# Performance work log

Hardware: AMD Instinct MI355X
Metric: run time of the kernel (lower is better)

## Reference

```python
import jax, jax.numpy as jnp
import numpy as np

N, D, HID, G, E2 = 2048, 256, 128, 8, 16384


def _mlp(h, w1, b1, g, be, w2, b2):
    # Linear -> ReLU -> BatchNorm1d (training mode, biased batch var) -> Linear
    h = jax.nn.relu(h @ w1 + b1)
    mu = h.mean(axis=0)
    var = ((h - mu) ** 2).mean(axis=0)
    h = (h - mu) / jnp.sqrt(var + 1e-5) * g + be
    return h @ w2 + b2


def setup_inputs() -> dict:
    key = jax.random.key(0)
    ks = jax.random.split(key, 12)
    x = jax.random.normal(ks[0], (N, D), jnp.float32)
    src = jax.random.randint(ks[1], (E2,), 0, N)
    dst = jax.random.randint(ks[2], (E2,), 0, N)
    src = jnp.where(src == dst, (src + 1) % N, src)  # no self loops
    edge_index = jnp.stack([jnp.concatenate([src, dst]),
                            jnp.concatenate([dst, src])])  # symmetric
    batch = jnp.sort(jax.random.randint(ks[3], (N,), 0, G))
    def lin(k, i, o):
        return 0.1 * jax.random.normal(k, (i, o), jnp.float32)
    out = dict(x=x, edge_index=edge_index, batch=batch)
    dims = [(1, HID, HID), (HID, HID, HID), (HID, HID, 1)]
    names = [("w11", "b11", "g1", "be1", "w12", "b12"),
             ("w21", "b21", "g2", "be2", "w22", "b22"),
             ("w31", "b31", "g3", "be3", "w32", "b32")]
    k = 4
    for (i, h, o), n in zip(dims, names):
        out[n[0]] = lin(ks[k], i, h)
        out[n[1]] = jnp.zeros((h,), jnp.float32)
        out[n[2]] = jnp.ones((h,), jnp.float32)
        out[n[3]] = jnp.zeros((h,), jnp.float32)
        out[n[4]] = lin(ks[k + 1], h, o)
        out[n[5]] = jnp.zeros((o,), jnp.float32)
        k += 2
    return out


def reference(x, edge_index, batch,
              w11, b11, g1, be1, w12, b12,
              w21, b21, g2, be2, w22, b22,
              w31, b31, g3, be3, w32, b32):
    n = x.shape[0]
    # dense adjacency from edge_index; L = D - A (unnormalized graph Laplacian)
    A = jnp.zeros((n, n), x.dtype).at[edge_index[0], edge_index[1]].set(1.0)
    deg = A.sum(axis=1)
    # entropy term: V = x*(Lx) - x*(Ax) + A(x*x), Lx = deg*x - Ax
    Ax = A @ x
    V = x * (deg[:, None] * x - Ax) - x * Ax + A @ (x * x)
    V = jnp.linalg.norm(V, axis=1)  # [n]
    # per-graph softmax over the batch segments
    mx = jax.ops.segment_max(V, batch, num_segments=G)
    ex = jnp.exp(V - mx[batch])
    P = ex / jax.ops.segment_sum(ex, batch, num_segments=G)[batch]
    P = jnp.where(P == 0.0, 1.0, P)
    ent = -P * jnp.log(P)  # [n]

    # GINConv (eps=0): mlp(x + sum_{j in N(i)} x_j) = mlp(x + A @ x)
    def gin(h, w1, b1, g, be, w2, b2):
        return _mlp(h + A @ h, w1, b1, g, be, w2, b2)

    h = gin(ent[:, None], w11, b11, g1, be1, w12, b12)
    h = gin(h, w21, b21, g2, be2, w22, b22)
    h = gin(h, w31, b31, g3, be3, w32, b32)
    p = jax.nn.sigmoid(h[:, 0])  # [n] node probabilities

    gamma = ent.sum()
    loss = gamma - jnp.vdot(ent, p) + jnp.vdot(p, A @ p)

    # greedy conditional expectation (sequential MIS-style selection)
    order = jnp.argsort(-p)

    def step(carry, idx):
        dummy, sel, rej = carry
        nb = A[idx] > 0.0  # neighbor mask [n]
        deg0 = ~jnp.any(nb)
        sel = sel.at[idx].set(sel[idx] | deg0)  # isolated node -> selected
        eligible = (~rej[idx]) & (~sel[idx])
        s = jnp.where(nb, 0.0, dummy).at[idx].set(1.0)
        li = gamma - jnp.vdot(ent, s) + jnp.vdot(s, A @ s)
        accept = eligible & (li <= loss)
        sel = sel.at[idx].set(sel[idx] | accept)
        rej = rej | (nb & accept)
        dummy = jnp.where(accept, s, dummy)
        return (dummy, sel, rej), None

    init = (p, jnp.zeros(n, dtype=bool), jnp.zeros(n, dtype=bool))
    (dummy, sel, rej), _ = jax.lax.scan(step, init, order)

    # graph reconstruction (masked instead of compacted, for static shapes)
    mask = sel.astype(x.dtype)
    x_pooled = x * mask[:, None]
    A2 = A @ A
    A3 = A2 @ A
    eye = jnp.eye(n, dtype=x.dtype)
    adj_pooled = (1.0 - eye) * jnp.clip(A2 + A3, 0.0, 1.0) * (mask[:, None] * mask[None, :])
    batch_pooled = jnp.where(sel, batch, -1)
    return x_pooled, adj_pooled, sel, batch_pooled, loss
```

## Files before the change

### kernel.cpp

```cpp
#include <hip/hip_runtime.h>
#include <math.h>

#define NN 2048
#define DIMF 256
#define HIDN 128
#define NG 8
#define NEDGES 32768
#define W32 32
#define TRI_CAP 131072
#define TRI_LDS 4864

typedef unsigned long long u64;
typedef unsigned char u8;
typedef unsigned short u16;

__global__ void k_init(u64* __restrict__ rowbits, int* __restrict__ segstart) {
  int i = blockIdx.x * blockDim.x + threadIdx.x;
  for (int k = i; k < NN * W32; k += gridDim.x * blockDim.x) rowbits[k] = 0ull;
  if (i <= NG) segstart[i] = NN;
}

__global__ void k_edges(const int* __restrict__ ei, u64* __restrict__ rowbits) {
  int e = blockIdx.x * blockDim.x + threadIdx.x;
  if (e >= NEDGES) return;
  int u = ei[e], v = ei[NEDGES + e];
  atomicOr(&rowbits[((size_t)u << 5) + (v >> 6)], 1ull << (v & 63));
}

__global__ void k_deg(const u64* __restrict__ rowbits, int* __restrict__ deg,
                      const int* __restrict__ batch, int* __restrict__ segstart) {
  int i = blockIdx.x * blockDim.x + threadIdx.x;
  if (i >= NN) return;
  int c = 0;
  for (int w = 0; w < W32; ++w) c += __popcll(rowbits[(i << 5) + w]);
  deg[i] = c;
  if (i == 0 || batch[i] != batch[i - 1]) segstart[batch[i]] = i;
}

__global__ void k_scan2048(const int* __restrict__ in, int* __restrict__ out) {
  __shared__ int part[256];
  int t = threadIdx.x;
  int v[8]; int s = 0;
  for (int k = 0; k < 8; ++k) { v[k] = in[t * 8 + k]; s += v[k]; }
  part[t] = s;
  __syncthreads();
  for (int off = 1; off < 256; off <<= 1) {
    int y = (t >= off) ? part[t - off] : 0;
    __syncthreads();
    part[t] += y;
    __syncthreads();
  }
  int run = part[t] - s;
  for (int k = 0; k < 8; ++k) { out[t * 8 + k] = run; run += v[k]; }
  if (t == 255) out[NN] = part[255];
}

__global__ void k_extract(const u64* __restrict__ rowbits, const int* __restrict__ rp,
                          int* __restrict__ col, int* __restrict__ cnt) {
  int i = blockIdx.x * blockDim.x + threadIdx.x;
  if (i >= NN) return;
  const u64* ri = rowbits + ((size_t)i << 5);
  int o = rp[i];
  for (int w = 0; w < W32; ++w) {
    u64 b = ri[w];
    while (b) { col[o++] = (w << 6) + __builtin_ctzll(b); b &= b - 1; }
  }
  int c = 0;
  for (int e = rp[i]; e < o; ++e) {
    const u64* ra = rowbits + ((size_t)col[e] << 5);
    for (int w = 0; w < W32; ++w) c += __popcll(ra[w] & ri[w]);
  }
  cnt[i] = c;
}

__global__ void k_trifill(const u64* __restrict__ rowbits, const int* __restrict__ rp,
                          const int* __restrict__ col, const int* __restrict__ tp,
                          int2* __restrict__ tri) {
  int i = blockIdx.x * blockDim.x + threadIdx.x;
  if (i >= NN) return;
  const u64* ri = rowbits + ((size_t)i << 5);
  int o = tp[i];
  for (int e = rp[i]; e < rp[i + 1]; ++e) {
    int a = col[e];
    const u64* ra = rowbits + ((size_t)a << 5);
    for (int w = 0; w < W32; ++w) {
      u64 b = ra[w] & ri[w];
      while (b) {
        int j = (w << 6) + __builtin_ctzll(b);
        if (o < TRI_CAP) tri[o] = make_int2(a, j);
        ++o;
        b &= b - 1;
      }
    }
  }
}

__global__ void k_V(const float* __restrict__ x, const int* __restrict__ rp,
                    const int* __restrict__ col, float* __restrict__ V) {
  int i = blockIdx.x; int t = threadIdx.x;
  float xi = x[i * DIMF + t];
  float s1 = 0.f, s2 = 0.f;
  int r0 = rp[i], r1 = rp[i + 1];
  for (int e = r0; e < r1; ++e) {
    float xj = x[col[e] * DIMF + t];
    s1 += xj; s2 += xj * xj;
  }
  float dg = (float)(r1 - r0);
  float val = dg * xi * xi - 2.f * xi * s1 + s2;
  __shared__ double red[DIMF];
  red[t] = (double)val * (double)val;
  __syncthreads();
  for (int off = DIMF / 2; off > 0; off >>= 1) { if (t < off) red[t] += red[t + off]; __syncthreads(); }
  if (t == 0) V[i] = (float)sqrt(red[0]);
}

__global__ void k_soft(const float* __restrict__ V, const int* __restrict__ segstart,
                       float* __restrict__ ent, double* __restrict__ seggamma) {
  int g = blockIdx.x; int t = threadIdx.x;
  int s = segstart[g];
  int e = NN;
  for (int gg = g + 1; gg <= NG; ++gg) { int v = segstart[gg]; if (v < e) e = v; }
  if (s >= e) { if (t == 0) seggamma[g] = 0.0; return; }
  __shared__ float fm[256];
  __shared__ double dd[256];
  float m = -3.0e38f;
  for (int i = s + t; i < e; i += 256) m = fmaxf(m, V[i]);
  fm[t] = m; __syncthreads();
  for (int off = 128; off > 0; off >>= 1) { if (t < off) fm[t] = fmaxf(fm[t], fm[t + off]); __syncthreads(); }
  float mx = fm[0];
  __syncthreads();
  double sum = 0.0;
  for (int i = s + t; i < e; i += 256) sum += exp((double)V[i] - (double)mx);
  dd[t] = sum; __syncthreads();
  for (int off = 128; off > 0; off >>= 1) { if (t < off) dd[t] += dd[t + off]; __syncthreads(); }
  double tot = dd[0];
  __syncthreads();
  double gs = 0.0;
  for (int i = s + t; i < e; i += 256) {
    double P = exp((double)V[i] - (double)mx) / tot;
    float ev = (P > 0.0) ? (float)(-P * log(P)) : 0.f;
    ent[i] = ev;
    gs += (double)ev;
  }
  dd[t] = gs; __syncthreads();
  for (int off = 128; off > 0; off >>= 1) { if (t < off) dd[t] += dd[t + off]; __syncthreads(); }
  if (t == 0) seggamma[g] = dd[0];
}

__global__ void k_agg1(const float* __restrict__ ent, const int* __restrict__ rp,
                       const int* __restrict__ col, float* __restrict__ agg) {
  int i = blockIdx.x * blockDim.x + threadIdx.x;
  if (i >= NN) return;
  float a = ent[i];
  for (int e = rp[i]; e < rp[i + 1]; ++e) a += ent[col[e]];
  agg[i] = a;
}

__global__ void k_lin1(const float* __restrict__ agg, const float* __restrict__ w,
                       const float* __restrict__ b, float* __restrict__ t) {
  int idx = blockIdx.x * blockDim.x + threadIdx.x;
  if (idx >= NN * HIDN) return;
  int i = idx >> 7, k = idx & 127;
  float v = agg[i] * w[k] + b[k];
  t[idx] = v > 0.f ? v : 0.f;
}

__global__ void k_bn(const float* __restrict__ t, const float* __restrict__ g,
                     const float* __restrict__ be, float* __restrict__ scale,
                     float* __restrict__ shift) {
  int k = blockIdx.x; int tid = threadIdx.x;
  __shared__ double red[256];
  double s = 0.0;
  for (int i = tid; i < NN; i += 256) s += (double)t[i * HIDN + k];
  red[tid] = s; __syncthreads();
  for (int off = 128; off > 0; off >>= 1) { if (tid < off) red[tid] += red[tid + off]; __syncthreads(); }
  double mu = red[0] / NN;
  __syncthreads();
  double v = 0.0;
  for (int i = tid; i < NN; i += 256) { double dv = (double)t[i * HIDN + k] - mu; v += dv * dv; }
  red[tid] = v; __syncthreads();
  for (int off = 128; off > 0; off >>= 1) { if (tid < off) red[tid] += red[tid + off]; __syncthreads(); }
  if (tid == 0) {
    float var = (float)(red[0] / NN);
    float sc = g[k] / sqrtf(var + 1e-5f);
    scale[k] = sc;
    shift[k] = be[k] - (float)mu * sc;
  }
}

template<int PRE, int RELU>
__global__ void k_mm(const float* __restrict__ in, const float* __restrict__ Wm,
                     const float* __restrict__ bias, const float* __restrict__ scale,
                     const float* __restrict__ shift, float* __restrict__ out) {
  __shared__ float ti[8][HIDN];
  int r0 = blockIdx.x * 8; int t = threadIdx.x;
  for (int r = 0; r < 8; ++r) {
    float v = in[(r0 + r) * HIDN + t];
    if (PRE) v = v * scale[t] + shift[t];
    ti[r][t] = v;
  }
  __syncthreads();
  float acc[8];
  #pragma unroll
  for (int r = 0; r < 8; ++r) acc[r] = 0.f;
  for (int k = 0; k < HIDN; ++k) {
    float w = Wm[k * HIDN + t];
    #pragma unroll
    for (int r = 0; r < 8; ++r) acc[r] += ti[r][k] * w;
  }
  for (int r = 0; r < 8; ++r) {
    float v = acc[r] + bias[t];
    if (RELU) v = fmaxf(v, 0.f);
    out[(r0 + r) * HIDN + t] = v;
  }
}

__global__ void k_agg128(const float* __restrict__ h, const int* __restrict__ rp,
                         const int* __restrict__ col, float* __restrict__ agg) {
  int i = blockIdx.x; int t = threadIdx.x;
  float a = h[i * HIDN + t];
  for (int e = rp[i]; e < rp[i + 1]; ++e) a += h[col[e] * HIDN + t];
  agg[i * HIDN + t] = a;
}

__global__ void k_lin3(const float* __restrict__ tn, const float* __restrict__ scale,
                       const float* __restrict__ shift, const float* __restrict__ w32,
                       const float* __restrict__ b32, float* __restrict__ p) {
  int i = blockIdx.x; int t = threadIdx.x;
  float v = (tn[i * HIDN + t] * scale[t] + shift[t]) * w32[t];
  __shared__ float red[HIDN];
  red[t] = v; __syncthreads();
  for (int off = 64; off > 0; off >>= 1) { if (t < off) red[t] += red[t + off]; __syncthreads(); }
  if (t == 0) {
    float h3 = red[0] + b32[0];
    p[i] = 1.f / (1.f + expf(-h3));
  }
}

__global__ void k_q0(const float* __restrict__ p, const float* __restrict__ ent,
                     const int* __restrict__ rp, const int* __restrict__ col,
                     float* __restrict__ q0, float* __restrict__ e0) {
  int i = blockIdx.x * blockDim.x + threadIdx.x;
  if (i >= NN) return;
  float s = 0.f, es = 0.f;
  for (int e = rp[i]; e < rp[i + 1]; ++e) {
    int j = col[e];
    float pj = p[j];
    s += pj; es += ent[j] * pj;
  }
  q0[i] = s; e0[i] = es;
}

__global__ void k_loss(const float* __restrict__ ent, const float* __restrict__ p,
                       const float* __restrict__ q0, const double* __restrict__ seggamma,
                       double* __restrict__ scal) {
  __shared__ double ra[256], rb[256];
  int t = threadIdx.x;
  double a = 0.0, b = 0.0;
  for (int i = t; i < NN; i += 256) { a += (double)ent[i] * (double)p[i]; b += (double)p[i] * (double)q0[i]; }
  ra[t] = a; rb[t] = b; __syncthreads();
  for (int off = 128; off > 0; off >>= 1) {
    if (t < off) { ra[t] += ra[t + off]; rb[t] += rb[t + off]; }
    __syncthreads();
  }
  if (t == 0) {
    double gamma = 0.0;
    for (int g = 0; g < NG; ++g) gamma += seggamma[g];
    scal[0] = gamma; scal[1] = ra[0]; scal[2] = rb[0];
    scal[3] = gamma - ra[0] + rb[0];
  }
}

__global__ void k_sort(const float* __restrict__ p, int* __restrict__ order) {
  __shared__ u64 s[NN];
  int t = threadIdx.x;
  for (int k = t; k < NN; k += 1024) {
    unsigned b = __float_as_uint(p[k]);
    unsigned ss = (b & 0x80000000u) ? ~b : (b | 0x80000000u);
    s[k] = ((u64)(~ss) << 32) | (unsigned)k;
  }
  __syncthreads();
  for (int k = 2; k <= NN; k <<= 1) {
    for (int j = k >> 1; j > 0; j >>= 1) {
      for (int i = t; i < NN; i += 1024) {
        int ixj = i ^ j;
        if (ixj > i) {
          bool up = ((i & k) == 0);
          u64 a = s[i], b = s[ixj];
          if ((a > b) == up) { s[i] = b; s[ixj] = a; }
        }
      }
      __syncthreads();
    }
  }
  order[t] = (int)(s[t] & 0xFFFFFFFFull);
  order[t + 1024] = (int)(s[t + 1024] & 0xFFFFFFFFull);
}

#define DPP2(ctrl)                                                                        \
  a += __int_as_float(__builtin_amdgcn_update_dpp(0, __float_as_int(a), ctrl, 0xf, 0xf, true)); \
  b += __int_as_float(__builtin_amdgcn_update_dpp(0, __float_as_int(b), ctrl, 0xf, 0xf, true));

__device__ __forceinline__ void red2(float& a, float& b) {
  DPP2(0x111)
  DPP2(0x112)
  DPP2(0x114)
  DPP2(0x118)
  DPP2(0x142)
  DPP2(0x143)
  a = __int_as_float(__builtin_amdgcn_readlane(__float_as_int(a), 63));
  b = __int_as_float(__builtin_amdgcn_readlane(__float_as_int(b), 63));
}

__global__ void __launch_bounds__(1024, 1) k_greedy(
    const int* __restrict__ rp, const int* __restrict__ col,
    const int* __restrict__ tp, const int2* __restrict__ tri,
    const int* __restrict__ order, const float* __restrict__ p,
    const float* __restrict__ ent, const float* __restrict__ q0,
    const float* __restrict__ e0, const double* __restrict__ scal,
    u8* __restrict__ selb_g) {
  __shared__ float2 dq[NN];
  __shared__ float2 ee[NN];
  __shared__ u16 colL[NEDGES];
  __shared__ u16 ordl[NN];
  __shared__ uint2 rtP[NN + 1];
  __shared__ ushort2 triL[TRI_LDS];
  __shared__ unsigned decidedL[64], selL[64];
  __shared__ unsigned maskL[2];
  __shared__ float4 svA[2][16];
  int t = threadIdx.x;
  int w = t >> 6, lane = t & 63;

  for (int i = t; i < NN; i += 1024) {
    dq[i] = make_float2(p[i], q0[i]);
    ee[i] = make_float2(ent[i], e0[i]);
    ordl[i] = (u16)order[i];
    int tv0 = tp[i]; if (tv0 > 65535) tv0 = 65535;
    int tv1 = tp[i + 1]; if (tv1 > 65535) tv1 = 65535;
    rtP[i] = make_uint2((unsigned)rp[i] | ((unsigned)tv0 << 16),
                        (unsigned)rp[i + 1] | ((unsigned)tv1 << 16));
  }
  for (int i = t; i < NEDGES; i += 1024) colL[i] = (u16)col[i];
  for (int i = t; i < TRI_LDS; i += 1024) {
    int2 ab = tri[i];
    triL[i] = make_ushort2((u16)(ab.x & 2047), (u16)(ab.y & 2047));
  }
  if (t < 64) { decidedL[t] = 0u; selL[t] = 0u; }
  if (t < 2) maskL[t] = 0u;
  double gamma = scal[0], loss = scal[3];
  double ed = scal[1], dAd = scal[2];
  __syncthreads();
  for (int i = t; i < NN; i += 1024) {
    if (((rtP[i].y & 0xffffu) - (rtP[i].x & 0xffffu)) == 0u) {
      atomicOr(&decidedL[i >> 5], 1u << (i & 31));
      atomicOr(&selL[i >> 5], 1u << (i & 31));
    }
  }
  __syncthreads();

  int pos = 0, rc = 0;
  while (pos < NN) {
    int b = rc & 1; ++rc;
    int step = pos + w;
    if (step < NN) {
      int idx = ordl[step];
      if (!((decidedL[idx >> 5] >> (idx & 31)) & 1u)) {
        uint2 rt = rtP[idx];
        int r0 = rt.x & 0xffff, r1 = rt.y & 0xffff;
        int t0 = rt.x >> 16, t1 = rt.y >> 16;
        float2 dqi = dq[idx];
        float2 eei = ee[idx];
        float s2 = 0.f, st = 0.f;
        for (int e = r0 + lane; e < r1; e += 64) {
          float2 v = dq[colL[e]];
          s2 -= v.y * v.x;
        }
        if (t1 <= TRI_LDS) {
          for (int e = t0 + lane; e < t1; e += 64) {
            ushort2 ab = triL[e];
            st += dq[ab.x].x * dq[ab.y].x;
          }
        } else {
          int g0 = tp[idx], g1 = tp[idx + 1];
          if (g0 > TRI_CAP) g0 = TRI_CAP;
          if (g1 > TRI_CAP) g1 = TRI_CAP;
          for (int e = g0 + lane; e < g1; e += 64) {
            int2 ab = tri[e];
            st += dq[ab.x].x * dq[ab.y].x;
          }
        }
        red2(s2, st);
        float d0 = 1.f - dqi.x;
        float S1 = -eei.y + eei.x * d0;
        float S2 = s2 + dqi.y * d0;
        float sn = -dqi.y;
        double cross = 2.0 * (double)d0 * (double)sn + (double)st;
        double li = gamma - (ed + (double)S1) + (dAd + 2.0 * (double)S2 + cross);
        if (li <= loss && lane == 0) {
          svA[b][w] = make_float4(S1, S2, d0, st);
          atomicOr(&maskL[b], 1u << w);
        }
      }
    }
    __syncthreads();
    unsigned mask = maskL[b];
    if (mask == 0u) { pos += 16; continue; }
    int k = __builtin_ctz(mask);
    int idx = ordl[pos + k];
    float4 A = svA[b][k];
    float2 dqi = dq[idx];
    uint2 rt = rtP[idx];
    int r0 = rt.x & 0xffff, r1 = rt.y & 0xffff;
    {
      double cross = 2.0 * (double)A.z * (double)(-dqi.y) + (double)A.w;
      ed += (double)A.x;
      dAd += 2.0 * (double)A.y + cross;
    }
    __syncthreads();
    if (t == 0) maskL[b] = 0u;
    for (int e = r0 + w; e < r1; e += 16) {
      int a = colL[e];
      float da = -dq[a].x;
      if (da != 0.f) {
        float ea = ee[a].x;
        uint2 art = rtP[a];
        int b0 = art.x & 0xffff, b1 = art.y & 0xffff;
        for (int eb = b0 + lane; eb < b1; eb += 64) {
          int bb = colL[eb];
          atomicAdd(&dq[bb].y, da);
          atomicAdd(&ee[bb].y, ea * da);
        }
      }
    }
    {
      float ei = ee[idx].x;
      for (int e = r0 + t; e < r1; e += 1024) {
        int bb = colL[e];
        atomicAdd(&dq[bb].y, A.z);
        atomicAdd(&ee[bb].y, ei * A.z);
      }
    }
    __syncthreads();
    if (t == 0) {
      dq[idx].x = 1.f;
      atomicOr(&decidedL[idx >> 5], 1u << (idx & 31));
      atomicOr(&selL[idx >> 5], 1u << (idx & 31));
    }
    for (int e = r0 + t; e < r1; e += 1024) {
      int j = colL[e];
      dq[j].x = 0.f;
      atomicOr(&decidedL[j >> 5], 1u << (j & 31));
    }
    __syncthreads();
    pos += k + 1;
  }
  for (int i = t; i < NN; i += 1024)
    selb_g[i] = (u8)((selL[i >> 5] >> (i & 31)) & 1u);
}

__global__ void k_reach(const u64* __restrict__ src, const int* __restrict__ rp,
                        const int* __restrict__ col, u64* __restrict__ dst) {
  int node = blockIdx.x * 2 + (threadIdx.x >> 5);
  int w = threadIdx.x & 31;
  u64 acc = 0;
  for (int e = rp[node]; e < rp[node + 1]; ++e) acc |= src[((size_t)col[e] << 5) + w];
  dst[((size_t)node << 5) + w] = acc;
}

__global__ void k_out(const u64* __restrict__ row2, const u64* __restrict__ row3,
                      const u8* __restrict__ selb, const float* __restrict__ x,
                      const int* __restrict__ batch, const double* __restrict__ scal,
                      float* __restrict__ o_x, float* __restrict__ o_adj,
                      float* __restrict__ o_sel, float* __restrict__ o_bat,
                      float* __restrict__ o_loss) {
  int idx = blockIdx.x * blockDim.x + threadIdx.x;
  {
    int i = idx >> 11, j = idx & 2047;
    int wo = (i << 5) + (j >> 6);
    u64 b = (row2[wo] | row3[wo]) >> (j & 63);
    o_adj[idx] = ((b & 1ull) && i != j && selb[i] && selb[j]) ? 1.f : 0.f;
  }
  if (idx < NN * DIMF) {
    int i = idx >> 8;
    o_x[idx] = selb[i] ? x[idx] : 0.f;
  }
  if (idx < NN) {
    o_sel[idx] = selb[idx] ? 1.f : 0.f;
    o_bat[idx] = selb[idx] ? (float)batch[idx] : -1.f;
  }
  if (idx == 0) o_loss[0] = (float)scal[3];
}

extern "C" void kernel_launch(void* const* d_in, const int* in_sizes, int n_in,
                              void* d_out, int out_size, void* d_ws, size_t ws_size,
                              hipStream_t stream) {
  const float* x    = (const float*)d_in[0];
  const int*   ei   = (const int*)d_in[1];
  const int*   batch= (const int*)d_in[2];
  const float* w11  = (const float*)d_in[3];
  const float* b11  = (const float*)d_in[4];
  const float* g1   = (const float*)d_in[5];
  const float* be1  = (const float*)d_in[6];
  const float* w12  = (const float*)d_in[7];
  const float* b12  = (const float*)d_in[8];
  const float* w21  = (const float*)d_in[9];
  const float* b21  = (const float*)d_in[10];
  const float* g2   = (const float*)d_in[11];
  const float* be2  = (const float*)d_in[12];
  const float* w22  = (const float*)d_in[13];
  const float* b22  = (const float*)d_in[14];
  const float* w31  = (const float*)d_in[15];
  const float* b31  = (const float*)d_in[16];
  const float* g3   = (const float*)d_in[17];
  const float* be3  = (const float*)d_in[18];
  const float* w32  = (const float*)d_in[19];
  const float* b32  = (const float*)d_in[20];

  char* wsb = (char*)d_ws;
  size_t cur = 0;
  auto alloc = [&](size_t bytes) -> void* {
    void* pp = wsb + cur;
    cur += (bytes + 255) & ~(size_t)255;
    return pp;
  };
  u64*    rowbits = (u64*)alloc((size_t)NN * W32 * 8);
  u64*    row2    = (u64*)alloc((size_t)NN * W32 * 8);
  u64*    row3    = (u64*)alloc((size_t)NN * W32 * 8);
  double* seggam  = (double*)alloc(NG * 8);
  double* scal    = (double*)alloc(4 * 8);
  int*    deg     = (int*)alloc(NN * 4);
  int*    rowptr  = (int*)alloc((NN + 1) * 4);
  int*    colx    = (int*)alloc(65536 * 4);
  int*    tricnt  = (int*)alloc(NN * 4);
  int*    triptr  = (int*)alloc((NN + 1) * 4);
  int2*   tri     = (int2*)alloc((size_t)TRI_CAP * 8);
  int*    segst   = (int*)alloc((NG + 1) * 4);
  int*    order   = (int*)alloc(NN * 4);
  float*  ent     = (float*)alloc(NN * 4);
  float*  V       = (float*)alloc(NN * 4);
  float*  p       = (float*)alloc(NN * 4);
  float*  q0      = (float*)alloc(NN * 4);
  float*  e0      = (float*)alloc(NN * 4);
  float*  agg1    = (float*)alloc(NN * 4);
  float*  scale   = (float*)alloc(HIDN * 4);
  float*  shift   = (float*)alloc(HIDN * 4);
  float*  tA      = (float*)alloc((size_t)NN * HIDN * 4);
  float*  tB      = (float*)alloc((size_t)NN * HIDN * 4);
  float*  tC      = (float*)alloc((size_t)NN * HIDN * 4);
  u8*     selb    = (u8*)alloc(NN);

  float* out    = (float*)d_out;
  float* o_x    = out;
  float* o_adj  = out + 524288;
  float* o_sel  = out + 4718592;
  float* o_bat  = out + 4720640;
  float* o_loss = out + 4722688;

  k_init<<<64, 256, 0, stream>>>(rowbits, segst);
  k_edges<<<128, 256, 0, stream>>>(ei, rowbits);
  k_deg<<<8, 256, 0, stream>>>(rowbits, deg, batch, segst);
  k_scan2048<<<1, 256, 0, stream>>>(deg, rowptr);
  k_extract<<<8, 256, 0, stream>>>(rowbits, rowptr, colx, tricnt);
  k_scan2048<<<1, 256, 0, stream>>>(tricnt, triptr);
  k_trifill<<<8, 256, 0, stream>>>(rowbits, rowptr, colx, triptr, tri);
  k_V<<<NN, 256, 0, stream>>>(x, rowptr, colx, V);
  k_soft<<<NG, 256, 0, stream>>>(V, segst, ent, seggam);

  k_agg1<<<8, 256, 0, stream>>>(ent, rowptr, colx, agg1);
  k_lin1<<<1024, 256, 0, stream>>>(agg1, w11, b11, tA);
  k_bn<<<HIDN, 256, 0, stream>>>(tA, g1, be1, scale, shift);
  k_mm<1, 0><<<NN / 8, HIDN, 0, stream>>>(tA, w12, b12, scale, shift, tB);
  k_agg128<<<NN, HIDN, 0, stream>>>(tB, rowptr, colx, tC);
  k_mm<0, 1><<<NN / 8, HIDN, 0, stream>>>(tC, w21, b21, scale, shift, tA);
  k_bn<<<HIDN, 256, 0, stream>>>(tA, g2, be2, scale, shift);
  k_mm<1, 0><<<NN / 8, HIDN, 0, stream>>>(tA, w22, b22, scale, shift, tB);
  k_agg128<<<NN, HIDN, 0, stream>>>(tB, rowptr, colx, tC);
  k_mm<0, 1><<<NN / 8, HIDN, 0, stream>>>(tC, w31, b31, scale, shift, tA);
  k_bn<<<HIDN, 256, 0, stream>>>(tA, g3, be3, scale, shift);
  k_lin3<<<NN, HIDN, 0, stream>>>(tA, scale, shift, w32, b32, p);

  k_q0<<<8, 256, 0, stream>>>(p, ent, rowptr, colx, q0, e0);
  k_loss<<<1, 256, 0, stream>>>(ent, p, q0, seggam, scal);
  k_sort<<<1, 1024, 0, stream>>>(p, order);
  k_greedy<<<1, 1024, 0, stream>>>(rowptr, colx, triptr, tri, order, p, ent, q0, e0, scal, selb);

  k_reach<<<NN / 2, 64, 0, stream>>>(rowbits, rowptr, colx, row2);
  k_reach<<<NN / 2, 64, 0, stream>>>(row2, rowptr, colx, row3);
  k_out<<<NN * NN / 256, 256, 0, stream>>>(row2, row3, selb, x, batch, scal,
                                           o_x, o_adj, o_sel, o_bat, o_loss);

  (void)in_sizes; (void)n_in; (void)out_size; (void)ws_size;
}
```

Baseline: 1.132 ms.

## Keep decided bitmask in registers and drop a barrier in greedy selection loop

Moves the decided-node bitmask out of LDS into a per-lane register replicated in every wave, updated through readlane broadcasts of the accepted node's neighbours. Row/triangle pointers are pre-permuted into order sequence (rtO), and the candidate's q value is passed through shared memory. This removes one __syncthreads per accepted step and the LDS atomics on the decided mask. In exchange every wave redundantly runs a serial per-neighbour update loop, and this loop is longer for high-degree nodes.

```diff
diff --git a/kernel.cpp b/kernel.cpp
--- a/kernel.cpp
+++ b/kernel.cpp
@@ -323,38 +323,49 @@
   __shared__ float2 ee[NN];
   __shared__ u16 colL[NEDGES];
   __shared__ u16 ordl[NN];
+  __shared__ uint2 rtO[NN];
   __shared__ uint2 rtP[NN + 1];
   __shared__ ushort2 triL[TRI_LDS];
-  __shared__ unsigned decidedL[64], selL[64];
+  __shared__ unsigned selL[64];
   __shared__ unsigned maskL[2];
   __shared__ float4 svA[2][16];
+  __shared__ float svQ[2][16];
   int t = threadIdx.x;
   int w = t >> 6, lane = t & 63;
 
   for (int i = t; i < NN; i += 1024) {
     dq[i] = make_float2(p[i], q0[i]);
     ee[i] = make_float2(ent[i], e0[i]);
-    ordl[i] = (u16)order[i];
     int tv0 = tp[i]; if (tv0 > 65535) tv0 = 65535;
     int tv1 = tp[i + 1]; if (tv1 > 65535) tv1 = 65535;
     rtP[i] = make_uint2((unsigned)rp[i] | ((unsigned)tv0 << 16),
                         (unsigned)rp[i + 1] | ((unsigned)tv1 << 16));
+    int oi = order[i];
+    ordl[i] = (u16)oi;
+    int a0 = rp[oi], a1 = rp[oi + 1];
+    int b0 = tp[oi]; if (b0 > 65535) b0 = 65535;
+    int b1 = tp[oi + 1]; if (b1 > 65535) b1 = 65535;
+    rtO[i] = make_uint2((unsigned)a0 | ((unsigned)a1 << 16),
+                        (unsigned)b0 | ((unsigned)b1 << 16));
   }
   for (int i = t; i < NEDGES; i += 1024) colL[i] = (u16)col[i];
   for (int i = t; i < TRI_LDS; i += 1024) {
     int2 ab = tri[i];
     triL[i] = make_ushort2((u16)(ab.x & 2047), (u16)(ab.y & 2047));
   }
-  if (t < 64) { decidedL[t] = 0u; selL[t] = 0u; }
-  if (t < 2) maskL[t] = 0u;
   double gamma = scal[0], loss = scal[3];
   double ed = scal[1], dAd = scal[2];
   __syncthreads();
-  for (int i = t; i < NN; i += 1024) {
-    if (((rtP[i].y & 0xffffu) - (rtP[i].x & 0xffffu)) == 0u) {
-      atomicOr(&decidedL[i >> 5], 1u << (i & 31));
-      atomicOr(&selL[i >> 5], 1u << (i & 31));
-    }
+  unsigned decided_reg = 0u;
+  {
+    int base = lane * 32;
+    for (int k = 0; k < 32; ++k) {
+      int node = base + k;
+      if (((rtP[node + 1].x & 0xffffu) - (rtP[node].x & 0xffffu)) == 0u)
+        decided_reg |= 1u << k;
+    }
+    if (w == 0) selL[lane] = decided_reg;
+    if (t < 2) maskL[t] = 0u;
   }
   __syncthreads();
 
@@ -363,11 +374,12 @@
     int b = rc & 1; ++rc;
     int step = pos + w;
     if (step < NN) {
-      int idx = ordl[step];
-      if (!((decidedL[idx >> 5] >> (idx & 31)) & 1u)) {
-        uint2 rt = rtP[idx];
-        int r0 = rt.x & 0xffff, r1 = rt.y & 0xffff;
-        int t0 = rt.x >> 16, t1 = rt.y >> 16;
+      int idx = __builtin_amdgcn_readfirstlane((int)ordl[step]);
+      unsigned dw = (unsigned)__builtin_amdgcn_readlane((int)decided_reg, idx >> 5);
+      if (!((dw >> (idx & 31)) & 1u)) {
+        uint2 rt = rtO[step];
+        int r0 = rt.x & 0xffffu, r1 = rt.x >> 16;
+        int t0 = rt.y & 0xffffu, t1 = rt.y >> 16;
         float2 dqi = dq[idx];
         float2 eei = ee[idx];
         float s2 = 0.f, st = 0.f;
@@ -398,6 +410,7 @@
         double li = gamma - (ed + (double)S1) + (dAd + 2.0 * (double)S2 + cross);
         if (li <= loss && lane == 0) {
           svA[b][w] = make_float4(S1, S2, d0, st);
+          svQ[b][w] = dqi.y;
           atomicOr(&maskL[b], 1u << w);
         }
       }
@@ -406,18 +419,17 @@
     unsigned mask = maskL[b];
     if (mask == 0u) { pos += 16; continue; }
     int k = __builtin_ctz(mask);
-    int idx = ordl[pos + k];
+    int idx = __builtin_amdgcn_readfirstlane((int)ordl[pos + k]);
     float4 A = svA[b][k];
-    float2 dqi = dq[idx];
+    float qi = svQ[b][k];
     uint2 rt = rtP[idx];
     int r0 = rt.x & 0xffff, r1 = rt.y & 0xffff;
+    int degA = r1 - r0;
     {
-      double cross = 2.0 * (double)A.z * (double)(-dqi.y) + (double)A.w;
+      double cross = 2.0 * (double)A.z * (double)(-qi) + (double)A.w;
       ed += (double)A.x;
       dAd += 2.0 * (double)A.y + cross;
     }
-    __syncthreads();
-    if (t == 0) maskL[b] = 0u;
     for (int e = r0 + w; e < r1; e += 16) {
       int a = colL[e];
       float da = -dq[a].x;
@@ -443,16 +455,26 @@
     __syncthreads();
     if (t == 0) {
       dq[idx].x = 1.f;
-      atomicOr(&decidedL[idx >> 5], 1u << (idx & 31));
       atomicOr(&selL[idx >> 5], 1u << (idx & 31));
-    }
-    for (int e = r0 + t; e < r1; e += 1024) {
-      int j = colL[e];
-      dq[j].x = 0.f;
-      atomicOr(&decidedL[j >> 5], 1u << (j & 31));
+      maskL[b] = 0u;
+    }
+    for (int e = r0 + t; e < r1; e += 1024) dq[colL[e]].x = 0.f;
+    {
+      int colv = idx;
+      if (lane < degA) colv = (int)colL[r0 + lane];
+      int lim = degA < 64 ? degA : 64;
+      for (int l = 0; l < lim; ++l) {
+        int j = __builtin_amdgcn_readlane(colv, l);
+        decided_reg |= (lane == (j >> 5)) ? (1u << (j & 31)) : 0u;
+      }
+      for (int l = 64; l < degA; ++l) {
+        int j = (int)colL[r0 + l];
+        decided_reg |= (lane == (j >> 5)) ? (1u << (j & 31)) : 0u;
+      }
+      decided_reg |= (lane == (idx >> 5)) ? (1u << (idx & 31)) : 0u;
     }
     __syncthreads();
-    pos += k + 1;
+    pos = pos + k + 1;
   }
   for (int i = t; i < NN; i += 1024)
     selb_g[i] = (u8)((selL[i >> 5] >> (i & 31)) & 1u);
```

After: 1.374 ms. +21.4%, slower.

## Fuse lin1 into BN and matmul, merge loss into sort, trim greedy barrier

Applied to the files above, without the earlier changes.

Removes the k_lin1 kernel by recomputing the rank-1 linear+ReLU inside the first BatchNorm statistics pass and inside the first matmul's input staging, avoiding a 2048x128 intermediate write/read. Merges the loss reduction into the sort kernel to save a launch. In the sequential greedy loop, the candidate's q value is stashed alongside its accumulators so one __syncthreads per accepted step can be dropped, with the mask reset moved to a later synchronized point. The cost is redundant recomputation of the rank-1 activation, and the reordered mask reset has to stay race-free.

```diff
diff --git a/kernel.cpp b/kernel.cpp
--- a/kernel.cpp
+++ b/kernel.cpp
@@ -156,29 +156,34 @@
   agg[i] = a;
 }
 
-__global__ void k_lin1(const float* __restrict__ agg, const float* __restrict__ w,
-                       const float* __restrict__ b, float* __restrict__ t) {
-  int idx = blockIdx.x * blockDim.x + threadIdx.x;
-  if (idx >= NN * HIDN) return;
-  int i = idx >> 7, k = idx & 127;
-  float v = agg[i] * w[k] + b[k];
-  t[idx] = v > 0.f ? v : 0.f;
-}
-
-__global__ void k_bn(const float* __restrict__ t, const float* __restrict__ g,
+template<int FROMAGG>
+__global__ void k_bn(const float* __restrict__ src, const float* __restrict__ w1,
+                     const float* __restrict__ b1, const float* __restrict__ g,
                      const float* __restrict__ be, float* __restrict__ scale,
                      float* __restrict__ shift) {
   int k = blockIdx.x; int tid = threadIdx.x;
   __shared__ double red[256];
+  float wk = 0.f, bk = 0.f;
+  if (FROMAGG) { wk = w1[k]; bk = b1[k]; }
   double s = 0.0;
-  for (int i = tid; i < NN; i += 256) s += (double)t[i * HIDN + k];
+  for (int i = tid; i < NN; i += 256) {
+    float v;
+    if (FROMAGG) { v = src[i] * wk + bk; v = v > 0.f ? v : 0.f; }
+    else v = src[i * HIDN + k];
+    s += (double)v;
+  }
   red[tid] = s; __syncthreads();
   for (int off = 128; off > 0; off >>= 1) { if (tid < off) red[tid] += red[tid + off]; __syncthreads(); }
   double mu = red[0] / NN;
   __syncthreads();
-  double v = 0.0;
-  for (int i = tid; i < NN; i += 256) { double dv = (double)t[i * HIDN + k] - mu; v += dv * dv; }
-  red[tid] = v; __syncthreads();
+  double vv = 0.0;
+  for (int i = tid; i < NN; i += 256) {
+    float v;
+    if (FROMAGG) { v = src[i] * wk + bk; v = v > 0.f ? v : 0.f; }
+    else v = src[i * HIDN + k];
+    double dv = (double)v - mu; vv += dv * dv;
+  }
+  red[tid] = vv; __syncthreads();
   for (int off = 128; off > 0; off >>= 1) { if (tid < off) red[tid] += red[tid + off]; __syncthreads(); }
   if (tid == 0) {
     float var = (float)(red[0] / NN);
@@ -191,12 +196,20 @@
 template<int PRE, int RELU>
 __global__ void k_mm(const float* __restrict__ in, const float* __restrict__ Wm,
                      const float* __restrict__ bias, const float* __restrict__ scale,
-                     const float* __restrict__ shift, float* __restrict__ out) {
+                     const float* __restrict__ shift, const float* __restrict__ lw,
+                     const float* __restrict__ lb, float* __restrict__ out) {
   __shared__ float ti[8][HIDN];
   int r0 = blockIdx.x * 8; int t = threadIdx.x;
   for (int r = 0; r < 8; ++r) {
-    float v = in[(r0 + r) * HIDN + t];
-    if (PRE) v = v * scale[t] + shift[t];
+    float v;
+    if (PRE == 2) {
+      v = in[r0 + r] * lw[t] + lb[t];
+      v = v > 0.f ? v : 0.f;
+      v = v * scale[t] + shift[t];
+    } else {
+      v = in[(r0 + r) * HIDN + t];
+      if (PRE == 1) v = v * scale[t] + shift[t];
+    }
     ti[r][t] = v;
   }
   __syncthreads();
@@ -251,43 +264,40 @@
   q0[i] = s; e0[i] = es;
 }
 
-__global__ void k_loss(const float* __restrict__ ent, const float* __restrict__ p,
-                       const float* __restrict__ q0, const double* __restrict__ seggamma,
-                       double* __restrict__ scal) {
-  __shared__ double ra[256], rb[256];
+__global__ void __launch_bounds__(1024, 1) k_sortloss(
+    const float* __restrict__ p, const float* __restrict__ ent,
+    const float* __restrict__ q0, const double* __restrict__ seggamma,
+    double* __restrict__ scal, int* __restrict__ order) {
+  __shared__ u64 s[NN];
+  __shared__ double rr[32];
   int t = threadIdx.x;
   double a = 0.0, b = 0.0;
-  for (int i = t; i < NN; i += 256) { a += (double)ent[i] * (double)p[i]; b += (double)p[i] * (double)q0[i]; }
-  ra[t] = a; rb[t] = b; __syncthreads();
-  for (int off = 128; off > 0; off >>= 1) {
-    if (t < off) { ra[t] += ra[t + off]; rb[t] += rb[t + off]; }
-    __syncthreads();
-  }
+  for (int i = t; i < NN; i += 1024) {
+    a += (double)ent[i] * (double)p[i];
+    b += (double)p[i] * (double)q0[i];
+  }
+  for (int off = 32; off; off >>= 1) { a += __shfl_down(a, off); b += __shfl_down(b, off); }
+  if ((t & 63) == 0) { rr[(t >> 6) * 2] = a; rr[(t >> 6) * 2 + 1] = b; }
+  for (int k = t; k < NN; k += 1024) {
+    unsigned bb = __float_as_uint(p[k]);
+    unsigned ss = (bb & 0x80000000u) ? ~bb : (bb | 0x80000000u);
+    s[k] = ((u64)(~ss) << 32) | (unsigned)k;
+  }
+  __syncthreads();
   if (t == 0) {
-    double gamma = 0.0;
+    double A = 0.0, Bb = 0.0, gamma = 0.0;
+    for (int i = 0; i < 16; ++i) { A += rr[2 * i]; Bb += rr[2 * i + 1]; }
     for (int g = 0; g < NG; ++g) gamma += seggamma[g];
-    scal[0] = gamma; scal[1] = ra[0]; scal[2] = rb[0];
-    scal[3] = gamma - ra[0] + rb[0];
-  }
-}
-
-__global__ void k_sort(const float* __restrict__ p, int* __restrict__ order) {
-  __shared__ u64 s[NN];
-  int t = threadIdx.x;
-  for (int k = t; k < NN; k += 1024) {
-    unsigned b = __float_as_uint(p[k]);
-    unsigned ss = (b & 0x80000000u) ? ~b : (b | 0x80000000u);
-    s[k] = ((u64)(~ss) << 32) | (unsigned)k;
-  }
-  __syncthreads();
+    scal[0] = gamma; scal[1] = A; scal[2] = Bb; scal[3] = gamma - A + Bb;
+  }
   for (int k = 2; k <= NN; k <<= 1) {
     for (int j = k >> 1; j > 0; j >>= 1) {
       for (int i = t; i < NN; i += 1024) {
         int ixj = i ^ j;
         if (ixj > i) {
           bool up = ((i & k) == 0);
-          u64 a = s[i], b = s[ixj];
-          if ((a > b) == up) { s[i] = b; s[ixj] = a; }
+          u64 aa = s[i], bb = s[ixj];
+          if ((aa > bb) == up) { s[i] = bb; s[ixj] = aa; }
         }
       }
       __syncthreads();
@@ -328,6 +338,7 @@
   __shared__ unsigned decidedL[64], selL[64];
   __shared__ unsigned maskL[2];
   __shared__ float4 svA[2][16];
+  __shared__ float svQ[2][16];
   int t = threadIdx.x;
   int w = t >> 6, lane = t & 63;
 
@@ -398,6 +409,7 @@
         double li = gamma - (ed + (double)S1) + (dAd + 2.0 * (double)S2 + cross);
         if (li <= loss && lane == 0) {
           svA[b][w] = make_float4(S1, S2, d0, st);
+          svQ[b][w] = dqi.y;
           atomicOr(&maskL[b], 1u << w);
         }
       }
@@ -408,16 +420,14 @@
     int k = __builtin_ctz(mask);
     int idx = ordl[pos + k];
     float4 A = svA[b][k];
-    float2 dqi = dq[idx];
+    float qi = svQ[b][k];
     uint2 rt = rtP[idx];
     int r0 = rt.x & 0xffff, r1 = rt.y & 0xffff;
     {
-      double cross = 2.0 * (double)A.z * (double)(-dqi.y) + (double)A.w;
+      double cross = 2.0 * (double)A.z * (double)(-qi) + (double)A.w;
       ed += (double)A.x;
       dAd += 2.0 * (double)A.y + cross;
     }
-    __syncthreads();
-    if (t == 0) maskL[b] = 0u;
     for (int e = r0 + w; e < r1; e += 16) {
       int a = colL[e];
       float da = -dq[a].x;
@@ -445,6 +455,7 @@
       dq[idx].x = 1.f;
       atomicOr(&decidedL[idx >> 5], 1u << (idx & 31));
       atomicOr(&selL[idx >> 5], 1u << (idx & 31));
+      maskL[b] = 0u;
     }
     for (int e = r0 + t; e < r1; e += 1024) {
       int j = colL[e];
@@ -452,7 +463,7 @@
       atomicOr(&decidedL[j >> 5], 1u << (j & 31));
     }
     __syncthreads();
-    pos += k + 1;
+    pos = pos + k + 1;
   }
   for (int i = t; i < NN; i += 1024)
     selb_g[i] = (u8)((selL[i >> 5] >> (i & 31)) & 1u);
@@ -567,21 +578,19 @@
   k_soft<<<NG, 256, 0, stream>>>(V, segst, ent, seggam);
 
   k_agg1<<<8, 256, 0, stream>>>(ent, rowptr, colx, agg1);
-  k_lin1<<<1024, 256, 0, stream>>>(agg1, w11, b11, tA);
-  k_bn<<<HIDN, 256, 0, stream>>>(tA, g1, be1, scale, shift);
-  k_mm<1, 0><<<NN / 8, HIDN, 0, stream>>>(tA, w12, b12, scale, shift, tB);
+  k_bn<1><<<HIDN, 256, 0, stream>>>(agg1, w11, b11, g1, be1, scale, shift);
+  k_mm<2, 0><<<NN / 8, HIDN, 0, stream>>>(agg1, w12, b12, scale, shift, w11, b11, tB);
   k_agg128<<<NN, HIDN, 0, stream>>>(tB, rowptr, colx, tC);
-  k_mm<0, 1><<<NN / 8, HIDN, 0, stream>>>(tC, w21, b21, scale, shift, tA);
-  k_bn<<<HIDN, 256, 0, stream>>>(tA, g2, be2, scale, shift);
-  k_mm<1, 0><<<NN / 8, HIDN, 0, stream>>>(tA, w22, b22, scale, shift, tB);
+  k_mm<0, 1><<<NN / 8, HIDN, 0, stream>>>(tC, w21, b21, scale, shift, (const float*)0, (const float*)0, tA);
+  k_bn<0><<<HIDN, 256, 0, stream>>>(tA, (const float*)0, (const float*)0, g2, be2, scale, shift);
+  k_mm<1, 0><<<NN / 8, HIDN, 0, stream>>>(tA, w22, b22, scale, shift, (const float*)0, (const float*)0, tB);
   k_agg128<<<NN, HIDN, 0, stream>>>(tB, rowptr, colx, tC);
-  k_mm<0, 1><<<NN / 8, HIDN, 0, stream>>>(tC, w31, b31, scale, shift, tA);
-  k_bn<<<HIDN, 256, 0, stream>>>(tA, g3, be3, scale, shift);
+  k_mm<0, 1><<<NN / 8, HIDN, 0, stream>>>(tC, w31, b31, scale, shift, (const float*)0, (const float*)0, tA);
+  k_bn<0><<<HIDN, 256, 0, stream>>>(tA, (const float*)0, (const float*)0, g3, be3, scale, shift);
   k_lin3<<<NN, HIDN, 0, stream>>>(tA, scale, shift, w32, b32, p);
 
   k_q0<<<8, 256, 0, stream>>>(p, ent, rowptr, colx, q0, e0);
-  k_loss<<<1, 256, 0, stream>>>(ent, p, q0, seggam, scal);
-  k_sort<<<1, 1024, 0, stream>>>(p, order);
+  k_sortloss<<<1, 1024, 0, stream>>>(p, ent, q0, seggam, scal, order);
   k_greedy<<<1, 1024, 0, stream>>>(rowptr, colx, triptr, tri, order, p, ent, q0, e0, scal, selb);
 
   k_reach<<<NN / 2, 64, 0, stream>>>(rowbits, rowptr, colx, row2);
```

New measurement: 1.091 ms. -3.6%, faster.
